# Kernel tuning notes

Measured on AMD Instinct MI355X. Metric: run time of the kernel, lower is better.

The kernel has to match this reference:

```python
import jax, jax.numpy as jnp
import numpy as np

HID = 2048
NH = 16
HD = HID // NH
FF = 8192
SEQ = 2048
B = 1
EPS = 1e-05
ROPE_BASE = 10000.0


def _layernorm(x, w, b):
    mu = jnp.mean(x, axis=-1, keepdims=True)
    var = jnp.mean(jnp.square(x - mu), axis=-1, keepdims=True)
    return (x - mu) * jax.lax.rsqrt(var + EPS) * w + b


def _rope(x, offset):
    # x: [B, S, H, D]; rotate-half LLaMA-style rotary embedding
    S, D = x.shape[1], x.shape[3]
    inv_freq = 1.0 / (ROPE_BASE ** (jnp.arange(0, D, 2, dtype=jnp.float32) / D))  # [D/2]
    pos = jnp.arange(S, dtype=jnp.float32) + offset
    ang = pos[:, None] * inv_freq[None, :]                     # [S, D/2]
    cos = jnp.cos(ang)[None, :, None, :]                       # [1,S,1,D/2]
    sin = jnp.sin(ang)[None, :, None, :]
    x1, x2 = x[..., : D // 2], x[..., D // 2 :]
    return jnp.concatenate([x1 * cos - x2 * sin, x2 * cos + x1 * sin], axis=-1)


def setup_inputs() -> dict:
    key = jax.random.key(0)
    ks = jax.random.split(key, 16)
    sd = 0.02
    inp = {
        "hidden_states": jax.random.normal(ks[0], (B, SEQ, HID), dtype=jnp.float32),
        # additive causal mask as fed to multi_head_attention_forward
        "attention_mask": jnp.where(
            jnp.tril(jnp.ones((SEQ, SEQ), dtype=bool)), 0.0, -1e9
        ).astype(jnp.float32),
        "ln1_w": jnp.ones((HID,), jnp.float32),
        "ln1_b": jnp.zeros((HID,), jnp.float32),
        "ln2_w": jnp.ones((HID,), jnp.float32),
        "ln2_b": jnp.zeros((HID,), jnp.float32),
        "wq": jax.random.normal(ks[1], (HID, HID), jnp.float32) * sd,
        "bq": jnp.zeros((HID,), jnp.float32),
        "wk": jax.random.normal(ks[2], (HID, HID), jnp.float32) * sd,
        "bk": jnp.zeros((HID,), jnp.float32),
        "wv": jax.random.normal(ks[3], (HID, HID), jnp.float32) * sd,
        "bv": jnp.zeros((HID,), jnp.float32),
        "wo": jax.random.normal(ks[4], (HID, HID), jnp.float32) * sd,
        "bo": jnp.zeros((HID,), jnp.float32),
        "w_gate": jax.random.normal(ks[5], (FF, HID), jnp.float32) * sd,
        "w_up": jax.random.normal(ks[6], (FF, HID), jnp.float32) * sd,
        "w_down": jax.random.normal(ks[7], (HID, FF), jnp.float32) * sd,
        "total_seq_len": SEQ,
    }
    return inp


def reference(hidden_states, attention_mask, ln1_w, ln1_b, ln2_w, ln2_b,
              wq, bq, wk, bk, wv, bv, wo, bo, w_gate, w_up, w_down,
              total_seq_len):
    Bv, S, _ = hidden_states.shape
    x = _layernorm(hidden_states, ln1_w, ln1_b)
    q = (x @ wq.T + bq).reshape(Bv, S, NH, HD)
    k = (x @ wk.T + bk).reshape(Bv, S, NH, HD)
    v = (x @ wv.T + bv).reshape(Bv, S, NH, HD)
    offset = total_seq_len - S  # 0 for prefill
    q = _rope(q, offset)
    k = _rope(k, offset)
    # cache of max_sequence_length zeros concatenated with k/v then sliced to the
    # last total_seq_len entries == just the current k/v when total_seq_len == S
    scale = 1.0 / np.sqrt(HD)
    scores = jnp.einsum("bshd,bthd->bhst", q, k) * scale + attention_mask[None, None]
    probs = jax.nn.softmax(scores, axis=-1)
    attn = jnp.einsum("bhst,bthd->bshd", probs, v).reshape(Bv, S, HID)
    attn = attn @ wo.T + bo
    h = hidden_states + attn
    y = _layernorm(h, ln2_w, ln2_b)
    ffn = (jax.nn.silu(y @ w_gate.T) * (y @ w_up.T)) @ w_down.T
    return h + ffn
```

## Files before the change

kernel.cpp:

```cpp
#include <hip/hip_runtime.h>

#define HIDN 2048
#define NHEAD 16
#define HDIM 128
#define FFDIM 8192
#define SEQLEN 2048

typedef __attribute__((ext_vector_type(8))) __bf16 bf16x8;
typedef __attribute__((ext_vector_type(4))) float f32x4;
typedef __attribute__((ext_vector_type(4))) unsigned short u16x4;
typedef __attribute__((ext_vector_type(8))) unsigned short u16x8;

__device__ __forceinline__ unsigned short f2bfu(float f) {
    unsigned int u = __float_as_uint(f);
    unsigned int r = u + 0x7fffu + ((u >> 16) & 1u);
    return (unsigned short)(r >> 16);
}
__device__ __forceinline__ float bfu2f(unsigned short u) {
    return __uint_as_float(((unsigned int)u) << 16);
}

__device__ __forceinline__ void gload16(const void* g, void* l) {
    __builtin_amdgcn_global_load_lds(
        (const __attribute__((address_space(1))) unsigned int*)g,
        (__attribute__((address_space(3))) unsigned int*)l,
        16, 0, 0);
}

__global__ __launch_bounds__(256)
void conv_f32_bf16(const float* __restrict__ src, unsigned short* __restrict__ dst) {
    int i = blockIdx.x * 256 + threadIdx.x;
    float4 a = ((const float4*)src)[i * 2];
    float4 b = ((const float4*)src)[i * 2 + 1];
    u16x8 v;
    v[0] = f2bfu(a.x); v[1] = f2bfu(a.y); v[2] = f2bfu(a.z); v[3] = f2bfu(a.w);
    v[4] = f2bfu(b.x); v[5] = f2bfu(b.y); v[6] = f2bfu(b.z); v[7] = f2bfu(b.w);
    *(u16x8*)(dst + (size_t)i * 8) = v;
}

__global__ __launch_bounds__(256)
void conv3_f32_bf16(const float* __restrict__ s0, const float* __restrict__ s1,
                    const float* __restrict__ s2, unsigned short* __restrict__ dst) {
    int i = blockIdx.x * 256 + threadIdx.x;
    int m = i >> 19;
    int li = i & ((1 << 19) - 1);
    const float* s = (m == 0) ? s0 : (m == 1) ? s1 : s2;
    float4 a = ((const float4*)s)[li * 2];
    float4 b = ((const float4*)s)[li * 2 + 1];
    u16x8 v;
    v[0] = f2bfu(a.x); v[1] = f2bfu(a.y); v[2] = f2bfu(a.z); v[3] = f2bfu(a.w);
    v[4] = f2bfu(b.x); v[5] = f2bfu(b.y); v[6] = f2bfu(b.z); v[7] = f2bfu(b.w);
    *(u16x8*)(dst + (size_t)i * 8) = v;
}

__global__ __launch_bounds__(256)
void ln_bf16(const float* __restrict__ x, const float* __restrict__ w,
             const float* __restrict__ b, unsigned short* __restrict__ out) {
    const int row = blockIdx.x;
    const int tid = threadIdx.x;
    const float* xr = x + (size_t)row * HIDN;
    float4 v0 = ((const float4*)xr)[tid];
    float4 v1 = ((const float4*)xr)[tid + 256];
    float s = v0.x + v0.y + v0.z + v0.w + v1.x + v1.y + v1.z + v1.w;
    float q = v0.x*v0.x + v0.y*v0.y + v0.z*v0.z + v0.w*v0.w
            + v1.x*v1.x + v1.y*v1.y + v1.z*v1.z + v1.w*v1.w;
    for (int o = 32; o > 0; o >>= 1) {
        s += __shfl_down(s, o, 64);
        q += __shfl_down(q, o, 64);
    }
    __shared__ float red[8];
    const int wid = tid >> 6;
    if ((tid & 63) == 0) { red[wid] = s; red[4 + wid] = q; }
    __syncthreads();
    float st = red[0] + red[1] + red[2] + red[3];
    float qt = red[4] + red[5] + red[6] + red[7];
    float mu = st * (1.0f / HIDN);
    float var = qt * (1.0f / HIDN) - mu * mu;
    float rs = rsqrtf(var + 1e-5f);
    unsigned short* orow = out + (size_t)row * HIDN;
    int i0 = tid * 4, i1 = (tid + 256) * 4;
    orow[i0 + 0] = f2bfu((v0.x - mu) * rs * w[i0 + 0] + b[i0 + 0]);
    orow[i0 + 1] = f2bfu((v0.y - mu) * rs * w[i0 + 1] + b[i0 + 1]);
    orow[i0 + 2] = f2bfu((v0.z - mu) * rs * w[i0 + 2] + b[i0 + 2]);
    orow[i0 + 3] = f2bfu((v0.w - mu) * rs * w[i0 + 3] + b[i0 + 3]);
    orow[i1 + 0] = f2bfu((v1.x - mu) * rs * w[i1 + 0] + b[i1 + 0]);
    orow[i1 + 1] = f2bfu((v1.y - mu) * rs * w[i1 + 1] + b[i1 + 1]);
    orow[i1 + 2] = f2bfu((v1.z - mu) * rs * w[i1 + 2] + b[i1 + 2]);
    orow[i1 + 3] = f2bfu((v1.w - mu) * rs * w[i1 + 3] + b[i1 + 3]);
}

__global__ __launch_bounds__(256)
void wo_ln(const unsigned short* __restrict__ part, const float* __restrict__ h,
           const float* __restrict__ bo, const float* __restrict__ w,
           const float* __restrict__ b, float* __restrict__ out,
           unsigned short* __restrict__ ybf) {
    const int row = blockIdx.x;
    const int tid = threadIdx.x;
    const int c0 = tid * 4, c1 = (tid + 256) * 4;
    float4 o0 = ((const float4*)(h + (size_t)row * HIDN))[tid];
    float4 o1 = ((const float4*)(h + (size_t)row * HIDN))[tid + 256];
    o0.x += bo[c0]; o0.y += bo[c0 + 1]; o0.z += bo[c0 + 2]; o0.w += bo[c0 + 3];
    o1.x += bo[c1]; o1.y += bo[c1 + 1]; o1.z += bo[c1 + 2]; o1.w += bo[c1 + 3];
#pragma unroll
    for (int sk = 0; sk < 4; ++sk) {
        const unsigned short* pr = part + (size_t)sk * 4194304 + (size_t)row * HIDN;
        u16x4 p0 = *(const u16x4*)(pr + c0);
        u16x4 p1 = *(const u16x4*)(pr + c1);
        o0.x += bfu2f(p0[0]); o0.y += bfu2f(p0[1]); o0.z += bfu2f(p0[2]); o0.w += bfu2f(p0[3]);
        o1.x += bfu2f(p1[0]); o1.y += bfu2f(p1[1]); o1.z += bfu2f(p1[2]); o1.w += bfu2f(p1[3]);
    }
    ((float4*)(out + (size_t)row * HIDN))[tid] = o0;
    ((float4*)(out + (size_t)row * HIDN))[tid + 256] = o1;
    float s = o0.x + o0.y + o0.z + o0.w + o1.x + o1.y + o1.z + o1.w;
    float q = o0.x*o0.x + o0.y*o0.y + o0.z*o0.z + o0.w*o0.w
            + o1.x*o1.x + o1.y*o1.y + o1.z*o1.z + o1.w*o1.w;
    for (int o = 32; o > 0; o >>= 1) {
        s += __shfl_down(s, o, 64);
        q += __shfl_down(q, o, 64);
    }
    __shared__ float red[8];
    const int wid = tid >> 6;
    if ((tid & 63) == 0) { red[wid] = s; red[4 + wid] = q; }
    __syncthreads();
    float st = red[0] + red[1] + red[2] + red[3];
    float qt = red[4] + red[5] + red[6] + red[7];
    float mu = st * (1.0f / HIDN);
    float var = qt * (1.0f / HIDN) - mu * mu;
    float rs = rsqrtf(var + 1e-5f);
    unsigned short* yr = ybf + (size_t)row * HIDN;
    yr[c0 + 0] = f2bfu((o0.x - mu) * rs * w[c0 + 0] + b[c0 + 0]);
    yr[c0 + 1] = f2bfu((o0.y - mu) * rs * w[c0 + 1] + b[c0 + 1]);
    yr[c0 + 2] = f2bfu((o0.z - mu) * rs * w[c0 + 2] + b[c0 + 2]);
    yr[c0 + 3] = f2bfu((o0.w - mu) * rs * w[c0 + 3] + b[c0 + 3]);
    yr[c1 + 0] = f2bfu((o1.x - mu) * rs * w[c1 + 0] + b[c1 + 0]);
    yr[c1 + 1] = f2bfu((o1.y - mu) * rs * w[c1 + 1] + b[c1 + 1]);
    yr[c1 + 2] = f2bfu((o1.z - mu) * rs * w[c1 + 2] + b[c1 + 2]);
    yr[c1 + 3] = f2bfu((o1.w - mu) * rs * w[c1 + 3] + b[c1 + 3]);
}

__global__ __launch_bounds__(256)
void rope_kernel(unsigned short* __restrict__ qk, const int* __restrict__ tsl) {
    int id = blockIdx.x * 256 + threadIdx.x;
    int p  = id & 63;
    int hh = (id >> 6) & 31;
    int s  = id >> 11;
    int off = tsl[0] - SEQLEN;
    float inv = exp2f((float)p * -0.20762050593f);
    float ang = (float)(s + off) * inv;
    float c, sn;
    __sincosf(ang, &sn, &c);
    size_t base = (size_t)s * 4096 + hh * 128 + p;
    float x1 = bfu2f(qk[base]);
    float x2 = bfu2f(qk[base + 64]);
    qk[base]      = f2bfu(x1 * c - x2 * sn);
    qk[base + 64] = f2bfu(x2 * c + x1 * sn);
}

#define BAR asm volatile("s_barrier" ::: "memory")
#define VM4 asm volatile("s_waitcnt vmcnt(4)" ::: "memory")
#define VM0 asm volatile("s_waitcnt vmcnt(0)" ::: "memory")
#define LGK0 asm volatile("s_waitcnt lgkmcnt(0)" ::: "memory")

#define STAGE_A(tile, h) { const int k0_ = k_start + (tile) * 64;                      \
  _Pragma("unroll") for (int i_ = 0; i_ < 2; ++i_) {                                   \
    int d_ = (h) * 16384 + i_ * 8192 + tid * 16;                                       \
    int r_ = d_ >> 7;                                                                  \
    int cb_ = (d_ & 127) ^ ((r_ & 7) << 4);                                            \
    gload16((const char*)Ab + ((size_t)(brow + r_) * lda + k0_) * 2 + cb_,             \
            smem + ((tile) & 1) * 65536 + (h) * 16384 + i_ * 8192 + w * 1024); } }

#define STAGE_B(tile, h) { const int k0_ = k_start + (tile) * 64;                      \
  _Pragma("unroll") for (int i_ = 0; i_ < 2; ++i_) {                                   \
    int d_ = (h) * 16384 + i_ * 8192 + tid * 16;                                       \
    int r_ = d_ >> 7;                                                                  \
    int cb_ = (d_ & 127) ^ ((r_ & 7) << 4);                                            \
    gload16((const char*)Bb + ((size_t)(bcol + r_) * ldb + k0_) * 2 + cb_,             \
            smem + ((tile) & 1) * 65536 + 32768 + (h) * 16384 + i_ * 8192 + w * 1024); } }

#define LDB(BO)                                                                        \
  _Pragma("unroll") for (int n_ = 0; n_ < 4; ++n_)                                     \
  _Pragma("unroll") for (int kk_ = 0; kk_ < 2; ++kk_)                                  \
    bF[n_][kk_] = *(const bf16x8*)(smem + (BO) + bbase + n_ * 2048 + colb[kk_]);

#define LDA2(BO, MP)                                                                   \
  _Pragma("unroll") for (int dm_ = 0; dm_ < 2; ++dm_)                                  \
  _Pragma("unroll") for (int kk_ = 0; kk_ < 2; ++kk_)                                  \
    aF[dm_][kk_] = *(const bf16x8*)(smem + (BO) + abase + ((MP) * 2 + dm_) * 2048 + colb[kk_]);

#define MM(MP)                                                                         \
  __builtin_amdgcn_s_setprio(1);                                                       \
  _Pragma("unroll") for (int dm_ = 0; dm_ < 2; ++dm_)                                  \
  _Pragma("unroll") for (int n_ = 0; n_ < 4; ++n_)                                     \
  _Pragma("unroll") for (int kk_ = 0; kk_ < 2; ++kk_)                                  \
    acc[(MP) * 2 + dm_][n_] = __builtin_amdgcn_mfma_f32_16x16x32_bf16(                 \
        aF[dm_][kk_], bF[n_][kk_], acc[(MP) * 2 + dm_][n_], 0, 0, 0);                  \
  __builtin_amdgcn_s_setprio(0);

template<int EPI>
__global__ __launch_bounds__(512, 1)
void gemm256(const unsigned short* __restrict__ Ab, int lda,
             const unsigned short* __restrict__ Bb, int ldb,
             int k_len, int nbx, int ldc,
             const float* __restrict__ bias0, const float* __restrict__ bias1,
             const float* __restrict__ bias2,
             unsigned short* __restrict__ outB, unsigned short* __restrict__ outV) {
    extern __shared__ char smem[];
    const int tid = threadIdx.x;
    const int w = tid >> 6, lane = tid & 63;
    const int lr = lane & 15, lg = lane >> 4;
    const int wrow = (w >> 2) * 128;
    const int wc = w & 3;

    const int cpx = nbx >> 3;
    const int xcd = blockIdx.x & 7;
    const int loc = blockIdx.x >> 3;
    const int bx = xcd * cpx + loc % cpx;
    const int by = loc / cpx;
    const int brow = by * 256, bcol = bx * 256;
    const int k_start = blockIdx.y * k_len;

    const int xorv = (lr & 7) << 4;
    int colb[2];
    colb[0] = (lg * 16) ^ xorv;
    colb[1] = (64 + lg * 16) ^ xorv;
    const int abase = (wrow + lr) * 128;
    const int bbase = 32768 + (wc * 64 + lr) * 128;

    f32x4 acc[8][4];
#pragma unroll
    for (int m = 0; m < 8; ++m)
#pragma unroll
        for (int n = 0; n < 4; ++n) acc[m][n] = (f32x4){0.f, 0.f, 0.f, 0.f};

    bf16x8 bF[4][2], aF[2][2];

    const int NT = k_len >> 6;
    const int NIT = NT >> 1;

    STAGE_A(0, 0); STAGE_A(0, 1); STAGE_B(0, 0); STAGE_B(0, 1);
    STAGE_B(1, 0); STAGE_B(1, 1);
    VM4; BAR;

    for (int it = 0; it < NIT; ++it) {
        const int T = 2 * it;
        const bool s2 = (T + 2) < NT, s3 = (T + 3) < NT;
        LDB(0); LDA2(0, 0); STAGE_A(T + 1, 0); BAR; LGK0; MM(0); BAR;
        LDA2(0, 1); STAGE_A(T + 1, 1); BAR; LGK0; MM(1); BAR;
        LDA2(0, 2); if (s2) STAGE_B(T + 2, 0); BAR; LGK0; MM(2); BAR;
        LDA2(0, 3); if (s2) STAGE_B(T + 2, 1);
        if (s2) { VM4; } else { VM0; }
        BAR; LGK0; MM(3); BAR;
        LDB(65536); LDA2(65536, 0); if (s2) STAGE_A(T + 2, 0); BAR; LGK0; MM(0); BAR;
        LDA2(65536, 1); if (s2) STAGE_A(T + 2, 1); BAR; LGK0; MM(1); BAR;
        LDA2(65536, 2); if (s3) STAGE_B(T + 3, 0); BAR; LGK0; MM(2); BAR;
        LDA2(65536, 3); if (s3) STAGE_B(T + 3, 1);
        if (s3) { VM4; } else { VM0; }
        BAR; LGK0; MM(3); BAR;
    }

    char* sw = smem + w * 16384;
    const bool vblk = (EPI == 0) && (bcol >= 4096);

    if (!vblk) {
#pragma unroll
        for (int n = 0; n < 4; ++n) {
            const int col = bcol + wc * 64 + n * 16 + lr;
            float bv = 0.f;
            if (EPI == 0) bv = (col < 2048) ? bias0[col] : bias1[col - 2048];
#pragma unroll
            for (int m = 0; m < 8; ++m)
#pragma unroll
                for (int j = 0; j < 4; ++j) {
                    const int r = m * 16 + lg * 4 + j;
                    const int cb = ((n * 16 + lr) * 2) ^ ((r & 7) << 4);
                    *(unsigned short*)(sw + r * 128 + cb) = f2bfu(acc[m][n][j] + bv);
                }
        }
        const int rl = lane >> 3, cl = lane & 7;
#pragma unroll
        for (int it2 = 0; it2 < 16; ++it2) {
            const int r = it2 * 8 + rl;
            const int cb = (cl * 16) ^ ((r & 7) << 4);
            u16x8 val = *(const u16x8*)(sw + r * 128 + cb);
            const int gr = brow + wrow + r;
            const int gcol = bcol + wc * 64 + cl * 8;
            if (EPI == 0) {
                *(u16x8*)(outB + (size_t)gr * 4096 + gcol) = val;
            } else if (EPI == 1) {
                *(u16x8*)(outB + (size_t)gr * ldc + gcol) = val;
            } else if (EPI == 3) {
                unsigned short* gp = outB + (size_t)gr * ldc + gcol;
                u16x8 gv = *(const u16x8*)gp;
                u16x8 ov;
#pragma unroll
                for (int e = 0; e < 8; ++e) {
                    float g = bfu2f(gv[e]);
                    float uu = bfu2f(val[e]);
                    ov[e] = f2bfu(g / (1.0f + __expf(-g)) * uu);
                }
                *(u16x8*)gp = ov;
            } else {
                *(u16x8*)(outB + (size_t)blockIdx.y * 4194304 + (size_t)gr * ldc + gcol) = val;
            }
        }
    } else {
#pragma unroll
        for (int n = 0; n < 4; ++n) {
            const int c = n * 16 + lr;
            const float bv = bias2[bcol - 4096 + wc * 64 + c];
            const int cx = (c & 7) << 4;
#pragma unroll
            for (int m = 0; m < 8; ++m) {
                const int r0 = m * 16 + lg * 4;
                u16x4 pk;
#pragma unroll
                for (int j = 0; j < 4; ++j) pk[j] = f2bfu(acc[m][n][j] + bv);
                *(u16x4*)(sw + c * 256 + ((r0 * 2) ^ cx)) = pk;
            }
        }
        const int cg = lane >> 4, rl2 = lane & 15;
#pragma unroll
        for (int it2 = 0; it2 < 16; ++it2) {
            const int c = it2 * 4 + cg;
            const int rb = (rl2 * 16) ^ ((c & 7) << 4);
            u16x8 val = *(const u16x8*)(sw + c * 256 + rb);
            const int d = bcol - 4096 + wc * 64 + c;
            *(u16x8*)(outV + (size_t)d * SEQLEN + brow + wrow + rl2 * 8) = val;
        }
    }
}

__global__ __launch_bounds__(256)
void reduce4_add(const unsigned short* __restrict__ part, float* __restrict__ out) {
    int i = blockIdx.x * 256 + threadIdx.x;
    float4 o = ((const float4*)out)[i];
#pragma unroll
    for (int sk = 0; sk < 4; ++sk) {
        u16x4 p = ((const u16x4*)(part + (size_t)sk * 4194304))[i];
        o.x += bfu2f(p[0]); o.y += bfu2f(p[1]); o.z += bfu2f(p[2]); o.w += bfu2f(p[3]);
    }
    ((float4*)out)[i] = o;
}

#define PST 72
__global__ __launch_bounds__(256)
void attn_kernel(const unsigned short* __restrict__ QK, const unsigned short* __restrict__ VT,
                 unsigned short* __restrict__ O) {
    __shared__ __align__(16) unsigned short Ks[2][64 * 128];
    __shared__ __align__(16) unsigned short Vs[2][128 * 64];
    __shared__ __align__(16) unsigned short Ps[4][16 * PST];
    const int tid = threadIdx.x;
    const int lane = tid & 63;
    const int w = tid >> 6;
    const int lr = lane & 15, lg = lane >> 4;

    const int id = blockIdx.x;
    const int h = ((id & 7) << 1) | ((id >> 3) & 1);
    const int p = id >> 4;

    const unsigned short* Kb = QK + 2048 + h * 128;
    const unsigned short* Vb = VT + (size_t)(h * 128) * SEQLEN;

    int krow[4], kcb[4], vrow[4], vcb[4];
#pragma unroll
    for (int ch = 0; ch < 4; ++ch) {
        int d = ch * 4096 + w * 1024 + lane * 16;
        krow[ch] = d >> 8;
        kcb[ch]  = (d & 255) ^ ((krow[ch] & 7) << 4);
        vrow[ch] = d >> 7;
        vcb[ch]  = (d & 127) ^ ((vrow[ch] & 7) << 4);
    }

    const float sc = 0.08838834764831845f;

#pragma unroll 1
    for (int seg = 0; seg < 2; ++seg) {
        const int qb = seg ? (31 - p) : p;
        const int qw = qb * 64 + w * 16;
        const unsigned short* Qb = QK + (size_t)qw * 4096 + h * 128;

        bf16x8 qa[4];
#pragma unroll
        for (int c = 0; c < 4; ++c)
            qa[c] = *(const bf16x8*)(Qb + (size_t)lr * 4096 + c * 32 + lg * 8);

        f32x4 acc[8];
#pragma unroll
        for (int dt = 0; dt < 8; ++dt) acc[dt] = (f32x4){0.f, 0.f, 0.f, 0.f};
        float mrow[4] = {-INFINITY, -INFINITY, -INFINITY, -INFINITY};
        float lrow[4] = {0.f, 0.f, 0.f, 0.f};
        const int ntile = qb + 1;

#pragma unroll
        for (int ch = 0; ch < 4; ++ch) {
            gload16(Kb + (size_t)krow[ch] * 4096 + (kcb[ch] >> 1),
                    (char*)&Ks[0][0] + ch * 4096 + w * 1024);
            gload16(Vb + (size_t)vrow[ch] * SEQLEN + (vcb[ch] >> 1),
                    (char*)&Vs[0][0] + ch * 4096 + w * 1024);
        }
        __syncthreads();

        for (int tt = 0; tt < ntile; ++tt) {
            const int cur = tt & 1;
            const int t0 = tt * 64;
            if (tt + 1 < ntile) {
                const int t1 = t0 + 64;
#pragma unroll
                for (int ch = 0; ch < 4; ++ch) {
                    gload16(Kb + (size_t)(t1 + krow[ch]) * 4096 + (kcb[ch] >> 1),
                            (char*)&Ks[cur ^ 1][0] + ch * 4096 + w * 1024);
                    gload16(Vb + (size_t)vrow[ch] * SEQLEN + t1 + (vcb[ch] >> 1),
                            (char*)&Vs[cur ^ 1][0] + ch * 4096 + w * 1024);
                }
            }
            f32x4 s[4];
#pragma unroll
            for (int th = 0; th < 4; ++th) s[th] = (f32x4){0.f, 0.f, 0.f, 0.f};
            __builtin_amdgcn_s_setprio(1);
#pragma unroll
            for (int th = 0; th < 4; ++th) {
                const int row = th * 16 + lr;
#pragma unroll
                for (int c = 0; c < 4; ++c) {
                    bf16x8 kb = *(const bf16x8*)((char*)&Ks[cur][0] + row * 256 +
                                                 ((c * 64 + lg * 16) ^ ((lr & 7) << 4)));
                    s[th] = __builtin_amdgcn_mfma_f32_16x16x32_bf16(qa[c], kb, s[th], 0, 0, 0);
                }
            }
            __builtin_amdgcn_s_setprio(0);
#pragma unroll
            for (int th = 0; th < 4; ++th) {
                int tg = t0 + th * 16 + lr;
#pragma unroll
                for (int jj = 0; jj < 4; ++jj) {
                    int qg = qw + lg * 4 + jj;
                    s[th][jj] = s[th][jj] * sc + (tg <= qg ? 0.f : -1e9f);
                }
            }
            float mt[4];
#pragma unroll
            for (int jj = 0; jj < 4; ++jj)
                mt[jj] = fmaxf(fmaxf(s[0][jj], s[1][jj]), fmaxf(s[2][jj], s[3][jj]));
#pragma unroll
            for (int o = 8; o > 0; o >>= 1)
#pragma unroll
                for (int jj = 0; jj < 4; ++jj) mt[jj] = fmaxf(mt[jj], __shfl_xor(mt[jj], o, 16));
            bool need = false;
#pragma unroll
            for (int jj = 0; jj < 4; ++jj) need = need || (mt[jj] > mrow[jj] + 4.0f);
            if (__any(need)) {
#pragma unroll
                for (int jj = 0; jj < 4; ++jj) {
                    float mn = fmaxf(mrow[jj], mt[jj]);
                    float a = __expf(mrow[jj] - mn);
                    mrow[jj] = mn;
                    lrow[jj] *= a;
#pragma unroll
                    for (int dt = 0; dt < 8; ++dt) acc[dt][jj] *= a;
                }
            }
            float ps[4] = {0.f, 0.f, 0.f, 0.f};
#pragma unroll
            for (int th = 0; th < 4; ++th)
#pragma unroll
                for (int jj = 0; jj < 4; ++jj) {
                    float pp = __expf(s[th][jj] - mrow[jj]);
                    s[th][jj] = pp;
                    ps[jj] += pp;
                }
#pragma unroll
            for (int o = 8; o > 0; o >>= 1)
#pragma unroll
                for (int jj = 0; jj < 4; ++jj) ps[jj] += __shfl_xor(ps[jj], o, 16);
#pragma unroll
            for (int jj = 0; jj < 4; ++jj) lrow[jj] += ps[jj];
#pragma unroll
            for (int th = 0; th < 4; ++th)
#pragma unroll
                for (int jj = 0; jj < 4; ++jj)
                    Ps[w][(lg * 4 + jj) * PST + th * 16 + lr] = f2bfu(s[th][jj]);
            bf16x8 pa[2];
#pragma unroll
            for (int ks = 0; ks < 2; ++ks)
                pa[ks] = *(const bf16x8*)&Ps[w][lr * PST + ks * 32 + lg * 8];
            __builtin_amdgcn_s_setprio(1);
#pragma unroll
            for (int dt = 0; dt < 8; ++dt) {
                const int d = dt * 16 + lr;
#pragma unroll
                for (int ks = 0; ks < 2; ++ks) {
                    bf16x8 vb = *(const bf16x8*)((char*)&Vs[cur][0] + d * 128 +
                                                 ((ks * 64 + lg * 16) ^ ((lr & 7) << 4)));
                    acc[dt] = __builtin_amdgcn_mfma_f32_16x16x32_bf16(pa[ks], vb, acc[dt], 0, 0, 0);
                }
            }
            __builtin_amdgcn_s_setprio(0);
            __syncthreads();
        }
        float invl[4];
#pragma unroll
        for (int jj = 0; jj < 4; ++jj) invl[jj] = 1.0f / lrow[jj];
#pragma unroll
        for (int dt = 0; dt < 8; ++dt)
#pragma unroll
            for (int jj = 0; jj < 4; ++jj)
                O[(size_t)(qw + lg * 4 + jj) * HIDN + h * HDIM + dt * 16 + lr] =
                    f2bfu(acc[dt][jj] * invl[jj]);
    }
}

extern "C" void kernel_launch(void* const* d_in, const int* in_sizes, int n_in,
                              void* d_out, int out_size, void* d_ws, size_t ws_size,
                              hipStream_t stream) {
    const float* hidden = (const float*)d_in[0];
    const float* ln1w = (const float*)d_in[2];
    const float* ln1b = (const float*)d_in[3];
    const float* ln2w = (const float*)d_in[4];
    const float* ln2b = (const float*)d_in[5];
    const float* wq = (const float*)d_in[6];
    const float* bq = (const float*)d_in[7];
    const float* wk = (const float*)d_in[8];
    const float* bk = (const float*)d_in[9];
    const float* wv = (const float*)d_in[10];
    const float* bv = (const float*)d_in[11];
    const float* wo = (const float*)d_in[12];
    const float* bo = (const float*)d_in[13];
    const float* wg = (const float*)d_in[14];
    const float* wu = (const float*)d_in[15];
    const float* wd = (const float*)d_in[16];
    const int* tsl = (const int*)d_in[17];
    float* out = (float*)d_out;

    char* ws = (char*)d_ws;
    const size_t MB = 1024 * 1024;
    unsigned short* Wbuf = (unsigned short*)(ws);
    unsigned short* qk   = (unsigned short*)(ws + 32 * MB);
    unsigned short* vt   = (unsigned short*)(ws + 48 * MB);
    unsigned short* x_bf = (unsigned short*)(ws + 56 * MB);
    unsigned short* g_bf = (unsigned short*)(ws + 64 * MB);
    unsigned short* part = qk;
    unsigned short* y_bf = vt;

    const int HID2 = HIDN * HIDN;
    const int CONV_HID = HID2 / 8 / 256;
    const int CONV_FF  = FFDIM * HIDN / 8 / 256;
    const size_t LDSZ = 131072;

    conv3_f32_bf16<<<3 * CONV_HID, 256, 0, stream>>>(wq, wk, wv, Wbuf);
    ln_bf16<<<SEQLEN, 256, 0, stream>>>(hidden, ln1w, ln1b, x_bf);
    gemm256<0><<<dim3(192, 1), 512, LDSZ, stream>>>(x_bf, HIDN, Wbuf, HIDN, HIDN, 24, 0,
                                                    bq, bk, bv, qk, vt);
    rope_kernel<<<SEQLEN * 32 * 64 / 256, 256, 0, stream>>>(qk, tsl);
    attn_kernel<<<256, 256, 0, stream>>>(qk, vt, x_bf);

    conv_f32_bf16<<<CONV_HID, 256, 0, stream>>>(wo, Wbuf);
    gemm256<4><<<dim3(64, 4), 512, LDSZ, stream>>>(x_bf, HIDN, Wbuf, HIDN, 512, 8, HIDN,
                                                   nullptr, nullptr, nullptr, g_bf, nullptr);
    wo_ln<<<SEQLEN, 256, 0, stream>>>(g_bf, hidden, bo, ln2w, ln2b, out, y_bf);

    conv_f32_bf16<<<CONV_FF, 256, 0, stream>>>(wg, Wbuf);
    gemm256<1><<<dim3(256, 1), 512, LDSZ, stream>>>(y_bf, HIDN, Wbuf, HIDN, HIDN, 32, FFDIM,
                                                    nullptr, nullptr, nullptr, g_bf, nullptr);
    conv_f32_bf16<<<CONV_FF, 256, 0, stream>>>(wu, Wbuf);
    gemm256<3><<<dim3(256, 1), 512, LDSZ, stream>>>(y_bf, HIDN, Wbuf, HIDN, HIDN, 32, FFDIM,
                                                    nullptr, nullptr, nullptr, g_bf, nullptr);
    conv_f32_bf16<<<CONV_FF, 256, 0, stream>>>(wd, Wbuf);
    gemm256<4><<<dim3(64, 4), 512, LDSZ, stream>>>(g_bf, FFDIM, Wbuf, FFDIM, 2048, 8, HIDN,
                                                   nullptr, nullptr, nullptr, part, nullptr);
    reduce4_add<<<4096, 256, 0, stream>>>(part, out);
}
```

Measured before the change: 454.0 us.

## Triple-buffer A tiles in GEMM and drop per-phase LDS barriers

```diff
diff --git a/kernel.cpp b/kernel.cpp
--- a/kernel.cpp
+++ b/kernel.cpp
@@ -157,35 +157,34 @@
 }
 
 #define BAR asm volatile("s_barrier" ::: "memory")
-#define VM4 asm volatile("s_waitcnt vmcnt(4)" ::: "memory")
+#define VM8 asm volatile("s_waitcnt vmcnt(8)" ::: "memory")
 #define VM0 asm volatile("s_waitcnt vmcnt(0)" ::: "memory")
-#define LGK0 asm volatile("s_waitcnt lgkmcnt(0)" ::: "memory")
-
-#define STAGE_A(tile, h) { const int k0_ = k_start + (tile) * 64;                      \
+
+#define STAGE_A2(tile, h, OFF) { const int k0_ = k_start + (tile) * 64;                \
   _Pragma("unroll") for (int i_ = 0; i_ < 2; ++i_) {                                   \
     int d_ = (h) * 16384 + i_ * 8192 + tid * 16;                                       \
     int r_ = d_ >> 7;                                                                  \
     int cb_ = (d_ & 127) ^ ((r_ & 7) << 4);                                            \
     gload16((const char*)Ab + ((size_t)(brow + r_) * lda + k0_) * 2 + cb_,             \
-            smem + ((tile) & 1) * 65536 + (h) * 16384 + i_ * 8192 + w * 1024); } }
-
-#define STAGE_B(tile, h) { const int k0_ = k_start + (tile) * 64;                      \
+            smem + (OFF) + (h) * 16384 + i_ * 8192 + w * 1024); } }
+
+#define STAGE_B2(tile, h, OFF) { const int k0_ = k_start + (tile) * 64;                \
   _Pragma("unroll") for (int i_ = 0; i_ < 2; ++i_) {                                   \
     int d_ = (h) * 16384 + i_ * 8192 + tid * 16;                                       \
     int r_ = d_ >> 7;                                                                  \
     int cb_ = (d_ & 127) ^ ((r_ & 7) << 4);                                            \
     gload16((const char*)Bb + ((size_t)(bcol + r_) * ldb + k0_) * 2 + cb_,             \
-            smem + ((tile) & 1) * 65536 + 32768 + (h) * 16384 + i_ * 8192 + w * 1024); } }
-
-#define LDB(BO)                                                                        \
+            smem + (OFF) + (h) * 16384 + i_ * 8192 + w * 1024); } }
+
+#define LDB2(BO)                                                                       \
   _Pragma("unroll") for (int n_ = 0; n_ < 4; ++n_)                                     \
   _Pragma("unroll") for (int kk_ = 0; kk_ < 2; ++kk_)                                  \
     bF[n_][kk_] = *(const bf16x8*)(smem + (BO) + bbase + n_ * 2048 + colb[kk_]);
 
-#define LDA2(BO, MP)                                                                   \
+#define LDA2(AO, MP)                                                                   \
   _Pragma("unroll") for (int dm_ = 0; dm_ < 2; ++dm_)                                  \
   _Pragma("unroll") for (int kk_ = 0; kk_ < 2; ++kk_)                                  \
-    aF[dm_][kk_] = *(const bf16x8*)(smem + (BO) + abase + ((MP) * 2 + dm_) * 2048 + colb[kk_]);
+    aF[dm_][kk_] = *(const bf16x8*)(smem + (AO) + abase + ((MP) * 2 + dm_) * 2048 + colb[kk_]);
 
 #define MM(MP)                                                                         \
   __builtin_amdgcn_s_setprio(1);                                                       \
@@ -224,7 +223,7 @@
     colb[0] = (lg * 16) ^ xorv;
     colb[1] = (64 + lg * 16) ^ xorv;
     const int abase = (wrow + lr) * 128;
-    const int bbase = 32768 + (wc * 64 + lr) * 128;
+    const int bbase = (wc * 64 + lr) * 128;
 
     f32x4 acc[8][4];
 #pragma unroll
@@ -235,27 +234,23 @@
     bf16x8 bF[4][2], aF[2][2];
 
     const int NT = k_len >> 6;
-    const int NIT = NT >> 1;
-
-    STAGE_A(0, 0); STAGE_A(0, 1); STAGE_B(0, 0); STAGE_B(0, 1);
-    STAGE_B(1, 0); STAGE_B(1, 1);
-    VM4; BAR;
-
-    for (int it = 0; it < NIT; ++it) {
-        const int T = 2 * it;
-        const bool s2 = (T + 2) < NT, s3 = (T + 3) < NT;
-        LDB(0); LDA2(0, 0); STAGE_A(T + 1, 0); BAR; LGK0; MM(0); BAR;
-        LDA2(0, 1); STAGE_A(T + 1, 1); BAR; LGK0; MM(1); BAR;
-        LDA2(0, 2); if (s2) STAGE_B(T + 2, 0); BAR; LGK0; MM(2); BAR;
-        LDA2(0, 3); if (s2) STAGE_B(T + 2, 1);
-        if (s2) { VM4; } else { VM0; }
-        BAR; LGK0; MM(3); BAR;
-        LDB(65536); LDA2(65536, 0); if (s2) STAGE_A(T + 2, 0); BAR; LGK0; MM(0); BAR;
-        LDA2(65536, 1); if (s2) STAGE_A(T + 2, 1); BAR; LGK0; MM(1); BAR;
-        LDA2(65536, 2); if (s3) STAGE_B(T + 3, 0); BAR; LGK0; MM(2); BAR;
-        LDA2(65536, 3); if (s3) STAGE_B(T + 3, 1);
-        if (s3) { VM4; } else { VM0; }
-        BAR; LGK0; MM(3); BAR;
+    int aC = 0, aN = 32768, aP = 65536;
+    int bC = 98304, bN = 131072;
+
+    STAGE_A2(0, 0, aC); STAGE_A2(0, 1, aC); STAGE_B2(0, 0, bC); STAGE_B2(0, 1, bC);
+    STAGE_A2(1, 0, aN); STAGE_A2(1, 1, aN); STAGE_B2(1, 0, bN); STAGE_B2(1, 1, bN);
+    VM8; BAR;
+
+    for (int T = 0; T < NT; ++T) {
+        const bool sp = (T + 2) < NT;
+        LDB2(bC); LDA2(aC, 0); if (sp) STAGE_A2(T + 2, 0, aP); MM(0); BAR;
+        LDA2(aC, 1); if (sp) STAGE_A2(T + 2, 1, aP); MM(1); BAR;
+        LDA2(aC, 2); if (sp) STAGE_B2(T + 2, 0, bC); MM(2); BAR;
+        LDA2(aC, 3); if (sp) STAGE_B2(T + 2, 1, bC);
+        if (sp) { VM8; } else if (T + 2 == NT) { VM0; }
+        MM(3); BAR;
+        int t = aC; aC = aN; aN = aP; aP = t;
+        t = bC; bC = bN; bN = t;
     }
 
     char* sw = smem + w * 16384;
@@ -544,7 +539,7 @@
     const int HID2 = HIDN * HIDN;
     const int CONV_HID = HID2 / 8 / 256;
     const int CONV_FF  = FFDIM * HIDN / 8 / 256;
-    const size_t LDSZ = 131072;
+    const size_t LDSZ = 163840;
 
     conv3_f32_bf16<<<3 * CONV_HID, 256, 0, stream>>>(wq, wk, wv, Wbuf);
     ln_bf16<<<SEQLEN, 256, 0, stream>>>(hidden, ln1w, ln1b, x_bf);
```

Result: no change. 449.8 us (-0.9%).

## Overlap weight conversions with GEMM/attention blocks and trim GEMM barriers

Applied to the files above, without the earlier changes.

```diff
diff --git a/kernel.cpp b/kernel.cpp
--- a/kernel.cpp
+++ b/kernel.cpp
@@ -27,15 +27,23 @@
         16, 0, 0);
 }
 
+__device__ __forceinline__ void conv_groups(const float* __restrict__ src,
+                                            unsigned short* __restrict__ dst,
+                                            int i0, int stride, int n8) {
+    for (int i = i0; i < n8; i += stride) {
+        float4 a = ((const float4*)src)[i * 2];
+        float4 b = ((const float4*)src)[i * 2 + 1];
+        u16x8 v;
+        v[0] = f2bfu(a.x); v[1] = f2bfu(a.y); v[2] = f2bfu(a.z); v[3] = f2bfu(a.w);
+        v[4] = f2bfu(b.x); v[5] = f2bfu(b.y); v[6] = f2bfu(b.z); v[7] = f2bfu(b.w);
+        *(u16x8*)(dst + (size_t)i * 8) = v;
+    }
+}
+
 __global__ __launch_bounds__(256)
 void conv_f32_bf16(const float* __restrict__ src, unsigned short* __restrict__ dst) {
     int i = blockIdx.x * 256 + threadIdx.x;
-    float4 a = ((const float4*)src)[i * 2];
-    float4 b = ((const float4*)src)[i * 2 + 1];
-    u16x8 v;
-    v[0] = f2bfu(a.x); v[1] = f2bfu(a.y); v[2] = f2bfu(a.z); v[3] = f2bfu(a.w);
-    v[4] = f2bfu(b.x); v[5] = f2bfu(b.y); v[6] = f2bfu(b.z); v[7] = f2bfu(b.w);
-    *(u16x8*)(dst + (size_t)i * 8) = v;
+    conv_groups(src, dst, i, 1 << 30, i + 1);
 }
 
 __global__ __launch_bounds__(256)
@@ -156,10 +164,9 @@
     qk[base + 64] = f2bfu(x2 * c + x1 * sn);
 }
 
-#define BAR asm volatile("s_barrier" ::: "memory")
+#define BAR __builtin_amdgcn_s_barrier()
 #define VM4 asm volatile("s_waitcnt vmcnt(4)" ::: "memory")
 #define VM0 asm volatile("s_waitcnt vmcnt(0)" ::: "memory")
-#define LGK0 asm volatile("s_waitcnt lgkmcnt(0)" ::: "memory")
 
 #define STAGE_A(tile, h) { const int k0_ = k_start + (tile) * 64;                      \
   _Pragma("unroll") for (int i_ = 0; i_ < 2; ++i_) {                                   \
@@ -203,9 +210,20 @@
              int k_len, int nbx, int ldc,
              const float* __restrict__ bias0, const float* __restrict__ bias1,
              const float* __restrict__ bias2,
-             unsigned short* __restrict__ outB, unsigned short* __restrict__ outV) {
+             unsigned short* __restrict__ outB, unsigned short* __restrict__ outV,
+             int ngemm, const float* __restrict__ csrc,
+             unsigned short* __restrict__ cdst, int conv_n8) {
     extern __shared__ char smem[];
     const int tid = threadIdx.x;
+
+    if ((int)blockIdx.x >= ngemm) {
+        if (blockIdx.y == 0) {
+            const int nconv = gridDim.x - ngemm;
+            conv_groups(csrc, cdst, (blockIdx.x - ngemm) * 512 + tid, nconv * 512, conv_n8);
+        }
+        return;
+    }
+
     const int w = tid >> 6, lane = tid & 63;
     const int lr = lane & 15, lg = lane >> 4;
     const int wrow = (w >> 2) * 128;
@@ -244,18 +262,18 @@
     for (int it = 0; it < NIT; ++it) {
         const int T = 2 * it;
         const bool s2 = (T + 2) < NT, s3 = (T + 3) < NT;
-        LDB(0); LDA2(0, 0); STAGE_A(T + 1, 0); BAR; LGK0; MM(0); BAR;
-        LDA2(0, 1); STAGE_A(T + 1, 1); BAR; LGK0; MM(1); BAR;
-        LDA2(0, 2); if (s2) STAGE_B(T + 2, 0); BAR; LGK0; MM(2); BAR;
-        LDA2(0, 3); if (s2) STAGE_B(T + 2, 1);
+        LDB(0); LDA2(0, 0); STAGE_A(T + 1, 0); MM(0); BAR;
+        LDA2(0, 1); STAGE_A(T + 1, 1); MM(1); BAR;
+        LDA2(0, 2); if (s2) STAGE_B(T + 2, 0); MM(2); BAR;
+        LDA2(0, 3); if (s2) STAGE_B(T + 2, 1); MM(3);
         if (s2) { VM4; } else { VM0; }
-        BAR; LGK0; MM(3); BAR;
-        LDB(65536); LDA2(65536, 0); if (s2) STAGE_A(T + 2, 0); BAR; LGK0; MM(0); BAR;
-        LDA2(65536, 1); if (s2) STAGE_A(T + 2, 1); BAR; LGK0; MM(1); BAR;
-        LDA2(65536, 2); if (s3) STAGE_B(T + 3, 0); BAR; LGK0; MM(2); BAR;
-        LDA2(65536, 3); if (s3) STAGE_B(T + 3, 1);
+        BAR;
+        LDB(65536); LDA2(65536, 0); if (s2) STAGE_A(T + 2, 0); MM(0); BAR;
+        LDA2(65536, 1); if (s2) STAGE_A(T + 2, 1); MM(1); BAR;
+        LDA2(65536, 2); if (s3) STAGE_B(T + 3, 0); MM(2); BAR;
+        LDA2(65536, 3); if (s3) STAGE_B(T + 3, 1); MM(3);
         if (s3) { VM4; } else { VM0; }
-        BAR; LGK0; MM(3); BAR;
+        BAR;
     }
 
     char* sw = smem + w * 16384;
@@ -345,11 +363,20 @@
 #define PST 72
 __global__ __launch_bounds__(256)
 void attn_kernel(const unsigned short* __restrict__ QK, const unsigned short* __restrict__ VT,
-                 unsigned short* __restrict__ O) {
+                 unsigned short* __restrict__ O,
+                 const float* __restrict__ csrc, unsigned short* __restrict__ cdst,
+                 int conv_n8) {
     __shared__ __align__(16) unsigned short Ks[2][64 * 128];
     __shared__ __align__(16) unsigned short Vs[2][128 * 64];
     __shared__ __align__(16) unsigned short Ps[4][16 * PST];
     const int tid = threadIdx.x;
+
+    if ((int)blockIdx.x >= 256) {
+        const int nconv = gridDim.x - 256;
+        conv_groups(csrc, cdst, (blockIdx.x - 256) * 256 + tid, nconv * 256, conv_n8);
+        return;
+    }
+
     const int lane = tid & 63;
     const int w = tid >> 6;
     const int lr = lane & 15, lg = lane >> 4;
@@ -546,26 +573,39 @@
     const int CONV_FF  = FFDIM * HIDN / 8 / 256;
     const size_t LDSZ = 131072;
 
+    const bool big_ws = ws_size >= 128 * MB;
+    unsigned short* wgBuf = big_ws ? (unsigned short*)(ws + 96 * MB) : Wbuf;
+
     conv3_f32_bf16<<<3 * CONV_HID, 256, 0, stream>>>(wq, wk, wv, Wbuf);
     ln_bf16<<<SEQLEN, 256, 0, stream>>>(hidden, ln1w, ln1b, x_bf);
-    gemm256<0><<<dim3(192, 1), 512, LDSZ, stream>>>(x_bf, HIDN, Wbuf, HIDN, HIDN, 24, 0,
-                                                    bq, bk, bv, qk, vt);
+    gemm256<0><<<dim3(192 + 64, 1), 512, LDSZ, stream>>>(
+        x_bf, HIDN, Wbuf, HIDN, HIDN, 24, 0, bq, bk, bv, qk, vt,
+        192, wo, Wbuf + 3 * (size_t)HID2, HID2 / 8);
     rope_kernel<<<SEQLEN * 32 * 64 / 256, 256, 0, stream>>>(qk, tsl);
-    attn_kernel<<<256, 256, 0, stream>>>(qk, vt, x_bf);
-
-    conv_f32_bf16<<<CONV_HID, 256, 0, stream>>>(wo, Wbuf);
-    gemm256<4><<<dim3(64, 4), 512, LDSZ, stream>>>(x_bf, HIDN, Wbuf, HIDN, 512, 8, HIDN,
-                                                   nullptr, nullptr, nullptr, g_bf, nullptr);
+
+    if (big_ws) {
+        attn_kernel<<<512, 256, 0, stream>>>(qk, vt, x_bf, wg, wgBuf, FFDIM * HIDN / 8);
+    } else {
+        attn_kernel<<<256, 256, 0, stream>>>(qk, vt, x_bf, nullptr, nullptr, 0);
+    }
+
+    gemm256<4><<<dim3(64, 4), 512, LDSZ, stream>>>(
+        x_bf, HIDN, Wbuf + 3 * (size_t)HID2, HIDN, 512, 8, HIDN,
+        nullptr, nullptr, nullptr, g_bf, nullptr, 64, nullptr, nullptr, 0);
     wo_ln<<<SEQLEN, 256, 0, stream>>>(g_bf, hidden, bo, ln2w, ln2b, out, y_bf);
 
-    conv_f32_bf16<<<CONV_FF, 256, 0, stream>>>(wg, Wbuf);
-    gemm256<1><<<dim3(256, 1), 512, LDSZ, stream>>>(y_bf, HIDN, Wbuf, HIDN, HIDN, 32, FFDIM,
-                                                    nullptr, nullptr, nullptr, g_bf, nullptr);
+    if (!big_ws)
+        conv_f32_bf16<<<CONV_FF, 256, 0, stream>>>(wg, Wbuf);
+    gemm256<1><<<dim3(256, 1), 512, LDSZ, stream>>>(
+        y_bf, HIDN, wgBuf, HIDN, HIDN, 32, FFDIM,
+        nullptr, nullptr, nullptr, g_bf, nullptr, 256, nullptr, nullptr, 0);
     conv_f32_bf16<<<CONV_FF, 256, 0, stream>>>(wu, Wbuf);
-    gemm256<3><<<dim3(256, 1), 512, LDSZ, stream>>>(y_bf, HIDN, Wbuf, HIDN, HIDN, 32, FFDIM,
-                                                    nullptr, nullptr, nullptr, g_bf, nullptr);
+    gemm256<3><<<dim3(256, 1), 512, LDSZ, stream>>>(
+        y_bf, HIDN, Wbuf, HIDN, HIDN, 32, FFDIM,
+        nullptr, nullptr, nullptr, g_bf, nullptr, 256, nullptr, nullptr, 0);
     conv_f32_bf16<<<CONV_FF, 256, 0, stream>>>(wd, Wbuf);
-    gemm256<4><<<dim3(64, 4), 512, LDSZ, stream>>>(g_bf, FFDIM, Wbuf, FFDIM, 2048, 8, HIDN,
-                                                   nullptr, nullptr, nullptr, part, nullptr);
+    gemm256<4><<<dim3(64, 4), 512, LDSZ, stream>>>(
+        g_bf, FFDIM, Wbuf, FFDIM, 2048, 8, HIDN,
+        nullptr, nullptr, nullptr, part, nullptr, 64, nullptr, nullptr, 0);
     reduce4_add<<<4096, 256, 0, stream>>>(part, out);
 }
```

Result: faster. 430.2 us (-5.2%).
